# Optimization experiments

Hardware: AMD Instinct MI355X
Metric: run time of the kernel (lower is better)

## Reference

```python
import jax, jax.numpy as jnp
import numpy as np

SEQ, BSZ, D = 1024, 16, 512
HEADS = 8
DEG = 32
N = SEQ * BSZ
E = N * DEG
NEG_SLOPE = 0.2  # PyG GATConv leaky_relu slope


def setup_inputs() -> dict:
    key = jax.random.key(0)
    ks = jax.random.split(key, 12)
    x = jax.random.normal(ks[0], (SEQ, BSZ, D), dtype=jnp.float32)
    # per-graph random COO edges, node ids offset per graph (PyG Batch semantics)
    src = jax.random.randint(ks[1], (BSZ, SEQ * DEG), 0, SEQ)
    dst = jax.random.randint(ks[2], (BSZ, SEQ * DEG), 0, SEQ)
    off = (jnp.arange(BSZ) * SEQ)[:, None]
    edge_index = jnp.stack([(src + off).reshape(-1), (dst + off).reshape(-1)]).astype(jnp.int32)  # [2, E]
    s = 0.05
    W0 = jax.random.normal(ks[3], (D, D), dtype=jnp.float32) * s          # heads*64 = 512
    att_src0 = jax.random.normal(ks[4], (HEADS, 64), dtype=jnp.float32) * s
    att_dst0 = jax.random.normal(ks[5], (HEADS, 64), dtype=jnp.float32) * s
    b0 = jax.random.normal(ks[6], (D,), dtype=jnp.float32) * s
    W1 = jax.random.normal(ks[7], (D, HEADS * D), dtype=jnp.float32) * s  # concat=False layer
    att_src1 = jax.random.normal(ks[8], (HEADS, D), dtype=jnp.float32) * s
    att_dst1 = jax.random.normal(ks[9], (HEADS, D), dtype=jnp.float32) * s
    b1 = jax.random.normal(ks[10], (D,), dtype=jnp.float32) * s
    return {"x": x, "edge_index": edge_index, "W0": W0, "att_src0": att_src0,
            "att_dst0": att_dst0, "b0": b0, "W1": W1, "att_src1": att_src1,
            "att_dst1": att_dst1, "b1": b1}


def gat_conv(h_in, src, dst, n_nodes, W, a_src, a_dst, b, concat):
    """PyG GATConv (eval mode: no dropout). src/dst already include self-loops."""
    H, C = a_src.shape
    h = (h_in @ W).reshape(n_nodes, H, C)                     # [N,H,C]
    alpha_src = jnp.einsum('nhc,hc->nh', h, a_src)            # [N,H]
    alpha_dst = jnp.einsum('nhc,hc->nh', h, a_dst)
    e = jax.nn.leaky_relu(alpha_src[src] + alpha_dst[dst], NEG_SLOPE)  # [Etot,H]
    # segment softmax over incoming edges of each dst node
    m = jax.ops.segment_max(e, dst, num_segments=n_nodes)
    m = jnp.where(jnp.isfinite(m), m, 0.0)
    p = jnp.exp(e - m[dst])
    z = jax.ops.segment_sum(p, dst, num_segments=n_nodes)
    alpha = p / (z[dst] + 1e-16)                              # [Etot,H]
    msg = h[src] * alpha[:, :, None]                          # [Etot,H,C]
    out = jax.ops.segment_sum(msg, dst, num_segments=n_nodes) # [N,H,C]
    out = out.reshape(n_nodes, H * C) if concat else out.mean(axis=1)
    return out + b


def reference(x, edge_index, W0, att_src0, att_dst0, b0, W1, att_src1, att_dst1, b1):
    seq_len, bsz, d = x.shape
    n_nodes = seq_len * bsz
    # PyG Batch: graph n contributes x[:, n, :] as its node block
    nodes = jnp.transpose(x, (1, 0, 2)).reshape(n_nodes, d)
    # GATConv add_self_loops=True
    loop = jnp.arange(n_nodes, dtype=edge_index.dtype)
    src = jnp.concatenate([edge_index[0], loop])
    dst = jnp.concatenate([edge_index[1], loop])
    h = jax.nn.elu(gat_conv(nodes, src, dst, n_nodes, W0, att_src0, att_dst0, b0, concat=True))
    h = jax.nn.elu(gat_conv(h, src, dst, n_nodes, W1, att_src1, att_dst1, b1, concat=False))
    # original code: conv_x.view(seq_len, bsz, embed_dim)  (raw memory reinterpret)
    return h.reshape(seq_len, bsz, d)
```

## Files before the change

### kernel.cpp

```cpp
#include <hip/hip_runtime.h>
#include <hip/hip_bf16.h>


#define NNODES 16384

typedef unsigned short u16;
typedef unsigned int u32;
typedef __attribute__((ext_vector_type(8))) __bf16 bf16x8;
typedef __attribute__((ext_vector_type(4))) float f32x4;

__device__ __forceinline__ u16 f2bf(float v) {
    u32 u = __builtin_bit_cast(u32, v);
    u32 r = (u + 0x7fffu + ((u >> 16) & 1u)) >> 16;
    return (u16)r;
}
__device__ __forceinline__ float bf2f(u16 s) {
    u32 u = ((u32)s) << 16;
    return __builtin_bit_cast(float, u);
}
__device__ __forceinline__ float bflo(u32 u) {
    return __builtin_bit_cast(float, u << 16);
}
__device__ __forceinline__ float bfhi(u32 u) {
    return __builtin_bit_cast(float, u & 0xffff0000u);
}
__device__ __forceinline__ void split2(float v, u16& h, u16& l) {
    h = f2bf(v);
    l = f2bf(v - bf2f(h));
}
__device__ __forceinline__ u32 pack2(float a, float b) {
    return (u32)f2bf(a) | ((u32)f2bf(b) << 16);
}

__device__ __forceinline__ void gload_lds16(const u16* g, u16* l) {
    __builtin_amdgcn_global_load_lds(
        (__attribute__((address_space(1))) void*)(void*)(g),
        (__attribute__((address_space(3))) void*)(void*)(l), 16, 0, 0);
}

__global__ void zero_k(int* p, int n) {
    int i = blockIdx.x * 256 + threadIdx.x;
    if (i < n) p[i] = 0;
}

__global__ void count_k(const int* __restrict__ dst, int E, int* __restrict__ deg) {
    int i = blockIdx.x * 256 + threadIdx.x;
    if (i < E) atomicAdd(&deg[dst[i]], 1);
}

__global__ __launch_bounds__(1024) void scan_k(const int* __restrict__ deg,
                                               int* __restrict__ indptr,
                                               int* __restrict__ cursor, int n) {
    __shared__ int sums[1024];
    int t = threadIdx.x;
    int base = t * 16;
    int local[16];
    int s = 0;
    #pragma unroll
    for (int i = 0; i < 16; i++) { local[i] = s; s += deg[base + i]; }
    sums[t] = s;
    __syncthreads();
    for (int off = 1; off < 1024; off <<= 1) {
        int v = (t >= off) ? sums[t - off] : 0;
        __syncthreads();
        sums[t] += v;
        __syncthreads();
    }
    int base_sum = (t == 0) ? 0 : sums[t - 1];
    #pragma unroll
    for (int i = 0; i < 16; i++) {
        int v = base_sum + local[i];
        indptr[base + i] = v;
        cursor[base + i] = v;
    }
    if (t == 1023) indptr[n] = base_sum + s;
}

__global__ void scatter_k(const int* __restrict__ src, const int* __restrict__ dst,
                          int E, int* __restrict__ cursor, int* __restrict__ csr) {
    int i = blockIdx.x * 256 + threadIdx.x;
    if (i < E) {
        int pos = atomicAdd(&cursor[dst[i]], 1);
        csr[pos] = src[i];
    }
}

__global__ void prepx_k(const float* __restrict__ x, u16* __restrict__ xh,
                        u16* __restrict__ xl) {
    int idx = blockIdx.x * 256 + threadIdx.x;
    int e = idx << 2;
    int n = e >> 9, k = e & 511;
    int g = n >> 10, s = n & 1023;
    float4 v = *(const float4*)(x + ((size_t)(s * 16 + g) << 9) + k);
    u16 h[4], l[4];
    split2(v.x, h[0], l[0]);
    split2(v.y, h[1], l[1]);
    split2(v.z, h[2], l[2]);
    split2(v.w, h[3], l[3]);
    size_t o = ((size_t)n << 9) + k;
    *(ushort4*)(xh + o) = make_ushort4(h[0], h[1], h[2], h[3]);
    *(ushort4*)(xl + o) = make_ushort4(l[0], l[1], l[2], l[3]);
}

__global__ __launch_bounds__(256) void prepW0t_k(const float* __restrict__ W0,
                                                 u16* __restrict__ Wh,
                                                 u16* __restrict__ Wl) {
    __shared__ u32 tile[64][65];
    int b = blockIdx.x;
    int kt = (b >> 3) * 64, nt = (b & 7) * 64;
    int t = threadIdx.x;
    #pragma unroll
    for (int i = 0; i < 16; i++) {
        int idx = i * 256 + t;
        int r = idx >> 6, c = idx & 63;
        float v = W0[(size_t)(kt + r) * 512 + nt + c];
        u16 h, l;
        split2(v, h, l);
        tile[r][c] = ((u32)h << 16) | l;
    }
    __syncthreads();
    #pragma unroll
    for (int i = 0; i < 8; i++) {
        int idx = i * 256 + t;
        int r = idx >> 5, c2 = (idx & 31) * 2;
        u32 p0 = tile[c2][r], p1 = tile[c2 + 1][r];
        size_t o = (size_t)(nt + r) * 512 + kt + c2;
        *(ushort2*)(Wh + o) = make_ushort2((u16)(p0 >> 16), (u16)(p1 >> 16));
        *(ushort2*)(Wl + o) = make_ushort2((u16)(p0 & 0xffff), (u16)(p1 & 0xffff));
    }
}

__global__ __launch_bounds__(256) void prepW1t_k(const float* __restrict__ W1,
                                                 u16* __restrict__ Bh) {
    __shared__ u16 tile[64][66];
    int b = blockIdx.x;
    int hh = b >> 6;
    int rem = b & 63;
    int kt = (rem >> 3) * 64, ct = (rem & 7) * 64;
    int t = threadIdx.x;
    #pragma unroll
    for (int i = 0; i < 16; i++) {
        int idx = i * 256 + t;
        int r = idx >> 6, c = idx & 63;
        float v = W1[(size_t)(kt + r) * 4096 + hh * 512 + ct + c] * 0.125f;
        tile[r][c] = f2bf(v);
    }
    __syncthreads();
    #pragma unroll
    for (int i = 0; i < 8; i++) {
        int idx = i * 256 + t;
        int r = idx >> 5, c2 = (idx & 31) * 2;
        size_t o = (size_t)(ct + r) * 4096 + hh * 512 + kt + c2;
        *(ushort2*)(Bh + o) = make_ushort2(tile[c2][r], tile[c2 + 1][r]);
    }
}

template <int MODE, int TERMS>
__global__ __launch_bounds__(256) void mgemm_k(
    const u16* __restrict__ Ah, const u16* __restrict__ Al,
    const u16* __restrict__ Bh, const u16* __restrict__ Bl,
    void* __restrict__ Cv, int K, const float* __restrict__ bias,
    const float* __restrict__ att_s, const float* __restrict__ att_d,
    float* __restrict__ as_, float* __restrict__ ad_) {
    constexpr int pAl = 4096;
    constexpr int pBh = (TERMS == 3) ? 8192 : 4096;
    constexpr int pBl = 12288;
    constexpr int NSEG = (TERMS == 3) ? 8 : 4;
    __shared__ u16 smem[(TERMS == 3) ? 16384 : 8192];

    int t = threadIdx.x;
    int lane = t & 63, w = t >> 6;
    int wr = w >> 1, wc = w & 1;
    int row0 = blockIdx.y * 128, col0 = blockIdx.x * 128;

    f32x4 acc[4][4];
    #pragma unroll
    for (int i = 0; i < 4; i++)
        #pragma unroll
        for (int j = 0; j < 4; j++) acc[i][j] = (f32x4){0.f, 0.f, 0.f, 0.f};

    int srow = lane >> 2;
    int sl4 = lane & 3;
    const u16* gp[NSEG];
    u16* lp[NSEG];
    #pragma unroll
    for (int ii = 0; ii < NSEG; ii++) {
        int s = w * NSEG + ii;
        int pl = s >> 3, seg = s & 7;
        const u16* gb;
        int g0;
        if (TERMS == 3) {
            gb = (pl == 0) ? Ah : (pl == 1) ? Al : (pl == 2) ? Bh : Bl;
            g0 = (pl < 2) ? row0 : col0;
        } else {
            gb = (pl == 0) ? Ah : Bh;
            g0 = (pl == 0) ? row0 : col0;
        }
        int row = seg * 16 + srow;
        int slot = sl4 ^ ((row >> 1) & 3);
        gp[ii] = gb + (size_t)(g0 + row) * K + slot * 8;
        lp[ii] = smem + pl * 4096 + seg * 512;
    }

    int rl = lane & 15, kb = lane >> 4;

    for (int k0 = 0; k0 < K; k0 += 32) {
        #pragma unroll
        for (int ii = 0; ii < NSEG; ii++) gload_lds16(gp[ii] + k0, lp[ii]);
        __syncthreads();

        bf16x8 afh[4], afl_[4], bfh[4], bfl[4];
        #pragma unroll
        for (int f = 0; f < 4; f++) {
            int r = wr * 64 + f * 16 + rl;
            int off = r * 32 + ((kb ^ ((r >> 1) & 3)) << 3);
            afh[f] = *(const bf16x8*)(smem + off);
            if (TERMS == 3) afl_[f] = *(const bf16x8*)(smem + pAl + off);
        }
        #pragma unroll
        for (int j = 0; j < 4; j++) {
            int r = wc * 64 + j * 16 + rl;
            int off = r * 32 + ((kb ^ ((r >> 1) & 3)) << 3);
            bfh[j] = *(const bf16x8*)(smem + pBh + off);
            if (TERMS == 3) bfl[j] = *(const bf16x8*)(smem + pBl + off);
        }
        #pragma unroll
        for (int i = 0; i < 4; i++)
            #pragma unroll
            for (int j = 0; j < 4; j++) {
                if (TERMS == 3) {
                    acc[i][j] = __builtin_amdgcn_mfma_f32_16x16x32_bf16(
                        afl_[i], bfh[j], acc[i][j], 0, 0, 0);
                    acc[i][j] = __builtin_amdgcn_mfma_f32_16x16x32_bf16(
                        afh[i], bfl[j], acc[i][j], 0, 0, 0);
                }
                acc[i][j] = __builtin_amdgcn_mfma_f32_16x16x32_bf16(
                    afh[i], bfh[j], acc[i][j], 0, 0, 0);
            }
        __syncthreads();
    }

    int cr = kb * 4;
    #pragma unroll
    for (int i = 0; i < 4; i++) {
        #pragma unroll
        for (int j = 0; j < 4; j++) {
            int col = col0 + wc * 64 + j * 16 + rl;
            float bv = (MODE == 1) ? bias[col] : 0.f;
            f32x4 v = acc[i][j];
            #pragma unroll
            for (int q = 0; q < 4; q++) {
                float o = v[q] + bv;
                size_t grow = (size_t)(row0 + wr * 64 + i * 16 + cr + q);
                if (MODE == 1) {
                    o = o > 0.f ? o : __expf(o) - 1.f;
                    ((float*)Cv)[grow * 512 + col] = o;
                } else {
                    ((u16*)Cv)[grow * 512 + col] = f2bf(o);
                }
            }
        }
    }

    if (MODE == 2) {
        int h = (col0 >> 6) + wc;
        float as_v[4], ad_v[4];
        #pragma unroll
        for (int j = 0; j < 4; j++) {
            as_v[j] = att_s[h * 64 + j * 16 + rl];
            ad_v[j] = att_d[h * 64 + j * 16 + rl];
        }
        #pragma unroll
        for (int i = 0; i < 4; i++) {
            float ps[4] = {}, pd[4] = {};
            #pragma unroll
            for (int j = 0; j < 4; j++) {
                f32x4 v = acc[i][j];
                #pragma unroll
                for (int q = 0; q < 4; q++) {
                    ps[q] = fmaf(v[q], as_v[j], ps[q]);
                    pd[q] = fmaf(v[q], ad_v[j], pd[q]);
                }
            }
            #pragma unroll
            for (int off = 1; off < 16; off <<= 1) {
                #pragma unroll
                for (int q = 0; q < 4; q++) {
                    ps[q] += __shfl_xor(ps[q], off);
                    pd[q] += __shfl_xor(pd[q], off);
                }
            }
            if (rl == 0) {
                #pragma unroll
                for (int q = 0; q < 4; q++) {
                    size_t row = (size_t)(row0 + wr * 64 + i * 16 + cr + q);
                    as_[row * 8 + h] = ps[q];
                    ad_[row * 8 + h] = pd[q];
                }
            }
        }
    }
}

__global__ __launch_bounds__(256) void prep1_k(const float* __restrict__ W1,
                                               const float* __restrict__ as1,
                                               const float* __restrict__ ad1,
                                               float* __restrict__ ws1,
                                               float* __restrict__ wd1) {
    int k = blockIdx.x;
    int t = threadIdx.x;
    int h = t >> 5, lane = t & 31;
    float ps = 0.f, pd = 0.f;
    for (int c = lane; c < 512; c += 32) {
        float w = W1[(size_t)k * 4096 + h * 512 + c];
        ps += w * as1[h * 512 + c];
        pd += w * ad1[h * 512 + c];
    }
    #pragma unroll
    for (int off = 1; off < 32; off <<= 1) {
        ps += __shfl_xor(ps, off);
        pd += __shfl_xor(pd, off);
    }
    if (lane == 0) {
        ws1[k * 8 + h] = ps;
        wd1[k * 8 + h] = pd;
    }
}

__global__ __launch_bounds__(256) void node0w_k(
    const u16* __restrict__ h0b, const float* __restrict__ asrc,
    const float* __restrict__ adst, const int* __restrict__ indptr,
    const int* __restrict__ csr, const float* __restrict__ b0,
    const float* __restrict__ ws1, const float* __restrict__ wd1,
    u16* __restrict__ hl0b, float* __restrict__ as1, float* __restrict__ ad1) {
    int b = blockIdx.x;
    int wid = threadIdx.x >> 6;
    int l = threadIdx.x & 63;
    int d = (b & 7) * (NNODES / 8) + ((b >> 3) << 2) + wid;
    int h = l >> 3;
    int e0 = indptr[d];
    int ne = indptr[d + 1] - e0;
    float adh = adst[d * 8 + h];

    float m = -3.0e38f, z = 0.f;
    for (int e = (l & 7); e <= ne; e += 8) {
        int s = (e < ne) ? csr[e0 + e] : d;
        float v = asrc[s * 8 + h] + adh;
        v = v > 0.f ? v : 0.2f * v;
        float mn = fmaxf(m, v);
        z = z * __expf(m - mn) + __expf(v - mn);
        m = mn;
    }
    #pragma unroll
    for (int off = 1; off < 8; off <<= 1) {
        float mo = __shfl_xor(m, off);
        float zo = __shfl_xor(z, off);
        float mn = fmaxf(m, mo);
        z = z * __expf(m - mn) + zo * __expf(mo - mn);
        m = mn;
    }
    float rz = 1.0f / (z + 1e-16f);

    float acc[8] = {};
    for (int eb = 0; eb <= ne; eb += 8) {
        int idx = eb + (l & 7);
        int sv = (idx < ne) ? csr[e0 + idx] : d;
        int nn = min(8, ne + 1 - eb);
        #pragma unroll
        for (int i = 0; i < 8; i++) {
            if (i < nn) {
                int s = __shfl(sv, (l & 56) | i);
                float v = asrc[s * 8 + h] + adh;
                v = v > 0.f ? v : 0.2f * v;
                float a = __expf(v - m) * rz;
                int4 pv = *(const int4*)(h0b + ((size_t)s << 9) + 8 * l);
                acc[0] = fmaf(a, bflo(pv.x), acc[0]);
                acc[1] = fmaf(a, bfhi(pv.x), acc[1]);
                acc[2] = fmaf(a, bflo(pv.y), acc[2]);
                acc[3] = fmaf(a, bfhi(pv.y), acc[3]);
                acc[4] = fmaf(a, bflo(pv.z), acc[4]);
                acc[5] = fmaf(a, bfhi(pv.z), acc[5]);
                acc[6] = fmaf(a, bflo(pv.w), acc[6]);
                acc[7] = fmaf(a, bfhi(pv.w), acc[7]);
            }
        }
    }

    const float4* b4 = (const float4*)(b0 + 8 * l);
    float4 bva = b4[0], bvb = b4[1];
    float o[8];
    o[0] = acc[0] + bva.x; o[1] = acc[1] + bva.y;
    o[2] = acc[2] + bva.z; o[3] = acc[3] + bva.w;
    o[4] = acc[4] + bvb.x; o[5] = acc[5] + bvb.y;
    o[6] = acc[6] + bvb.z; o[7] = acc[7] + bvb.w;
    #pragma unroll
    for (int k = 0; k < 8; k++) o[k] = o[k] > 0.f ? o[k] : __expf(o[k]) - 1.f;
    int4 hv;
    hv.x = (int)pack2(o[0], o[1]);
    hv.y = (int)pack2(o[2], o[3]);
    hv.z = (int)pack2(o[4], o[5]);
    hv.w = (int)pack2(o[6], o[7]);
    *(int4*)(hl0b + ((size_t)d << 9) + 8 * l) = hv;

    float ps[8] = {}, pd[8] = {};
    #pragma unroll
    for (int k = 0; k < 8; k++) {
        const float4* w4 = (const float4*)(ws1 + (size_t)(8 * l + k) * 8);
        const float4* v4 = (const float4*)(wd1 + (size_t)(8 * l + k) * 8);
        float4 wa = w4[0], wb = w4[1];
        float4 va = v4[0], vb = v4[1];
        float ok = o[k];
        ps[0] = fmaf(ok, wa.x, ps[0]); ps[1] = fmaf(ok, wa.y, ps[1]);
        ps[2] = fmaf(ok, wa.z, ps[2]); ps[3] = fmaf(ok, wa.w, ps[3]);
        ps[4] = fmaf(ok, wb.x, ps[4]); ps[5] = fmaf(ok, wb.y, ps[5]);
        ps[6] = fmaf(ok, wb.z, ps[6]); ps[7] = fmaf(ok, wb.w, ps[7]);
        pd[0] = fmaf(ok, va.x, pd[0]); pd[1] = fmaf(ok, va.y, pd[1]);
        pd[2] = fmaf(ok, va.z, pd[2]); pd[3] = fmaf(ok, va.w, pd[3]);
        pd[4] = fmaf(ok, vb.x, pd[4]); pd[5] = fmaf(ok, vb.y, pd[5]);
        pd[6] = fmaf(ok, vb.z, pd[6]); pd[7] = fmaf(ok, vb.w, pd[7]);
    }
    #pragma unroll
    for (int off = 1; off < 64; off <<= 1) {
        #pragma unroll
        for (int j = 0; j < 8; j++) {
            ps[j] += __shfl_xor(ps[j], off);
            pd[j] += __shfl_xor(pd[j], off);
        }
    }
    #pragma unroll
    for (int j = 0; j < 8; j++) {
        if (l == j) as1[(size_t)d * 8 + j] = ps[j];
        if (l == 8 + j) ad1[(size_t)d * 8 + j] = pd[j];
    }
}

__global__ __launch_bounds__(256) void node1w_k(
    const u16* __restrict__ hl0b, const float* __restrict__ asrc,
    const float* __restrict__ adst, const int* __restrict__ indptr,
    const int* __restrict__ csr, u16* __restrict__ aggh, int base, int ch) {
    int b = blockIdx.x;
    int wid = threadIdx.x >> 6;
    int l = threadIdx.x & 63;
    int dl = (b & 7) * (ch >> 3) + ((b >> 3) << 2) + wid;
    int d = base + dl;
    int hme = l & 7;
    int e0 = indptr[d];
    int ne = indptr[d + 1] - e0;
    float adh = adst[d * 8 + hme];

    float m = -3.0e38f, z = 0.f;
    for (int e = (l >> 3); e <= ne; e += 8) {
        int s = (e < ne) ? csr[e0 + e] : d;
        float v = asrc[s * 8 + hme] + adh;
        v = v > 0.f ? v : 0.2f * v;
        float mn = fmaxf(m, v);
        z = z * __expf(m - mn) + __expf(v - mn);
        m = mn;
    }
    #pragma unroll
    for (int off = 8; off < 64; off <<= 1) {
        float mo = __shfl_xor(m, off);
        float zo = __shfl_xor(z, off);
        float mn = fmaxf(m, mo);
        z = z * __expf(m - mn) + zo * __expf(mo - mn);
        m = mn;
    }
    float rz = 1.0f / (z + 1e-16f);

    float acc[8][8] = {};
    for (int eb = 0; eb <= ne; eb += 8) {
        int idx = eb + (l & 7);
        int sv = (idx < ne) ? csr[e0 + idx] : d;
        int nn = min(8, ne + 1 - eb);
        #pragma unroll
        for (int i = 0; i < 8; i++) {
            if (i < nn) {
                int s = __shfl(sv, (l & 56) | i);
                float v = asrc[s * 8 + hme] + adh;
                v = v > 0.f ? v : 0.2f * v;
                float amine = __expf(v - m) * rz;
                float a[8];
                #pragma unroll
                for (int hh = 0; hh < 8; hh++)
                    a[hh] = __shfl(amine, (l & 56) | hh);
                int4 pv = *(const int4*)(hl0b + ((size_t)s << 9) + 8 * l);
                float f0 = bflo(pv.x), f1 = bfhi(pv.x);
                float f2 = bflo(pv.y), f3 = bfhi(pv.y);
                float f4 = bflo(pv.z), f5 = bfhi(pv.z);
                float f6 = bflo(pv.w), f7 = bfhi(pv.w);
                #pragma unroll
                for (int hh = 0; hh < 8; hh++) {
                    acc[hh][0] = fmaf(a[hh], f0, acc[hh][0]);
                    acc[hh][1] = fmaf(a[hh], f1, acc[hh][1]);
                    acc[hh][2] = fmaf(a[hh], f2, acc[hh][2]);
                    acc[hh][3] = fmaf(a[hh], f3, acc[hh][3]);
                    acc[hh][4] = fmaf(a[hh], f4, acc[hh][4]);
                    acc[hh][5] = fmaf(a[hh], f5, acc[hh][5]);
                    acc[hh][6] = fmaf(a[hh], f6, acc[hh][6]);
                    acc[hh][7] = fmaf(a[hh], f7, acc[hh][7]);
                }
            }
        }
    }

    #pragma unroll
    for (int hh = 0; hh < 8; hh++) {
        ushort4 qa = make_ushort4(f2bf(acc[hh][0]), f2bf(acc[hh][1]),
                                  f2bf(acc[hh][2]), f2bf(acc[hh][3]));
        ushort4 qb = make_ushort4(f2bf(acc[hh][4]), f2bf(acc[hh][5]),
                                  f2bf(acc[hh][6]), f2bf(acc[hh][7]));
        size_t ob = (size_t)dl * 4096 + hh * 512 + 8 * l;
        *(ushort4*)(aggh + ob) = qa;
        *(ushort4*)(aggh + ob + 4) = qb;
    }
}

extern "C" void kernel_launch(void* const* d_in, const int* in_sizes, int n_in,
                              void* d_out, int out_size, void* d_ws, size_t ws_size,
                              hipStream_t stream) {
    const float* x = (const float*)d_in[0];
    const int* ei = (const int*)d_in[1];
    const float* W0 = (const float*)d_in[2];
    const float* at_s0 = (const float*)d_in[3];
    const float* at_d0 = (const float*)d_in[4];
    const float* b0 = (const float*)d_in[5];
    const float* W1 = (const float*)d_in[6];
    const float* at_s1 = (const float*)d_in[7];
    const float* at_d1 = (const float*)d_in[8];
    const float* b1 = (const float*)d_in[9];
    float* out = (float*)d_out;

    const int N = NNODES;
    const int E = in_sizes[1] / 2;
    const int* esrc = ei;
    const int* edst = ei + E;

    char* p = (char*)d_ws;
    auto carve = [&](size_t bytes) -> void* {
        void* r = (void*)p;
        p += ((bytes + 255) & ~(size_t)255);
        return r;
    };
    u16* h0b = (u16*)carve((size_t)N * 512 * 2);
    u16* hl0b = (u16*)carve((size_t)N * 512 * 2);
    float* as0 = (float*)carve((size_t)N * 8 * 4);
    float* ad0 = (float*)carve((size_t)N * 8 * 4);
    float* as1 = (float*)carve((size_t)N * 8 * 4);
    float* ad1 = (float*)carve((size_t)N * 8 * 4);
    int* deg = (int*)carve((size_t)N * 4);
    int* indptr = (int*)carve((size_t)(N + 1) * 4);
    int* cursor = (int*)carve((size_t)N * 4);
    int* csr = (int*)carve((size_t)E * 4);
    float* ws1 = (float*)carve(512 * 8 * 4);
    float* wd1 = (float*)carve(512 * 8 * 4);
    u16* xh = (u16*)carve((size_t)N * 512 * 2);
    u16* xl = (u16*)carve((size_t)N * 512 * 2);
    u16* W0h = (u16*)carve((size_t)512 * 512 * 2);
    u16* W0l = (u16*)carve((size_t)512 * 512 * 2);
    u16* B1h = (u16*)carve((size_t)512 * 4096 * 2);
    size_t used = (size_t)(p - (char*)d_ws);

    int CH = 1024;
    const int cands[5] = {16384, 8192, 4096, 2048, 1024};
    for (int ci = 0; ci < 5; ci++) {
        if (ws_size >= used + (size_t)cands[ci] * 8192 + 512) {
            CH = cands[ci];
            break;
        }
    }
    u16* aggh = (u16*)carve((size_t)CH * 4096 * 2);

    zero_k<<<(N + 255) / 256, 256, 0, stream>>>(deg, N);
    count_k<<<(E + 255) / 256, 256, 0, stream>>>(edst, E, deg);
    scan_k<<<1, 1024, 0, stream>>>(deg, indptr, cursor, N);
    scatter_k<<<(E + 255) / 256, 256, 0, stream>>>(esrc, edst, E, cursor, csr);

    prepx_k<<<(N * 512 / 4 + 255) / 256, 256, 0, stream>>>(x, xh, xl);
    prepW0t_k<<<64, 256, 0, stream>>>(W0, W0h, W0l);
    prepW1t_k<<<512, 256, 0, stream>>>(W1, B1h);
    prep1_k<<<512, 256, 0, stream>>>(W1, at_s1, at_d1, ws1, wd1);

    mgemm_k<2, 3><<<dim3(4, N / 128), 256, 0, stream>>>(
        xh, xl, W0h, W0l, h0b, 512, nullptr, at_s0, at_d0, as0, ad0);
    node0w_k<<<N / 4, 256, 0, stream>>>(h0b, as0, ad0, indptr, csr, b0, ws1,
                                        wd1, hl0b, as1, ad1);

    for (int base = 0; base < N; base += CH) {
        node1w_k<<<CH / 4, 256, 0, stream>>>(hl0b, as1, ad1, indptr, csr, aggh,
                                             base, CH);
        mgemm_k<1, 1><<<dim3(4, CH / 128), 256, 0, stream>>>(
            aggh, nullptr, B1h, nullptr, out + (size_t)base * 512, 4096, b1,
            nullptr, nullptr, nullptr, nullptr);
    }
}
```

Measured before the change: 441.5 us.

## Remap GEMM blocks per XCD and double K-step for single-term path

The block index is remapped so that consecutive row-tiles land on the same XCD, with four column tiles sharing an A row-panel, to improve L2 reuse of A across the chiplet caches. The single-term (TERMS==1) path now loads 64 K-columns per iteration into the full 32KB shared buffer, halving the number of barriers and load rounds per tile. The remapping assumes gridDim.x==4 and gridDim.y divisible by 8. It also raises LDS use for the single-term kernel, which may reduce occupancy.

```diff
diff --git a/kernel.cpp b/kernel.cpp
--- a/kernel.cpp
+++ b/kernel.cpp
@@ -162,16 +162,17 @@
     void* __restrict__ Cv, int K, const float* __restrict__ bias,
     const float* __restrict__ att_s, const float* __restrict__ att_d,
     float* __restrict__ as_, float* __restrict__ ad_) {
-    constexpr int pAl = 4096;
-    constexpr int pBh = (TERMS == 3) ? 8192 : 4096;
-    constexpr int pBl = 12288;
-    constexpr int NSEG = (TERMS == 3) ? 8 : 4;
-    __shared__ u16 smem[(TERMS == 3) ? 16384 : 8192];
+    __shared__ u16 smem[16384];
 
     int t = threadIdx.x;
     int lane = t & 63, w = t >> 6;
     int wr = w >> 1, wc = w & 1;
-    int row0 = blockIdx.y * 128, col0 = blockIdx.x * 128;
+
+    int orig = blockIdx.x + (blockIdx.y << 2);
+    int xcd = orig & 7, slot = orig >> 3;
+    int by = xcd * ((int)gridDim.y >> 3) + (slot >> 2);
+    int bx = slot & 3;
+    int row0 = by * 128, col0 = bx * 128;
 
     f32x4 acc[4][4];
     #pragma unroll
@@ -181,63 +182,93 @@
 
     int srow = lane >> 2;
     int sl4 = lane & 3;
-    const u16* gp[NSEG];
-    u16* lp[NSEG];
-    #pragma unroll
-    for (int ii = 0; ii < NSEG; ii++) {
-        int s = w * NSEG + ii;
-        int pl = s >> 3, seg = s & 7;
+    const u16* gp[8];
+    u16* lp[8];
+    #pragma unroll
+    for (int ii = 0; ii < 8; ii++) {
         const u16* gb;
-        int g0;
+        int g0, koff;
         if (TERMS == 3) {
-            gb = (pl == 0) ? Ah : (pl == 1) ? Al : (pl == 2) ? Bh : Bl;
-            g0 = (pl < 2) ? row0 : col0;
+            gb = (w == 0) ? Ah : (w == 1) ? Al : (w == 2) ? Bh : Bl;
+            g0 = (w < 2) ? row0 : col0;
+            koff = 0;
         } else {
-            gb = (pl == 0) ? Ah : Bh;
-            g0 = (pl == 0) ? row0 : col0;
-        }
-        int row = seg * 16 + srow;
-        int slot = sl4 ^ ((row >> 1) & 3);
-        gp[ii] = gb + (size_t)(g0 + row) * K + slot * 8;
-        lp[ii] = smem + pl * 4096 + seg * 512;
+            gb = (w < 2) ? Ah : Bh;
+            g0 = (w < 2) ? row0 : col0;
+            koff = (w & 1) * 32;
+        }
+        int row = ii * 16 + srow;
+        int sslot = sl4 ^ ((row >> 1) & 3);
+        gp[ii] = gb + (size_t)(g0 + row) * K + koff + sslot * 8;
+        lp[ii] = smem + w * 4096 + ii * 512;
     }
 
     int rl = lane & 15, kb = lane >> 4;
 
-    for (int k0 = 0; k0 < K; k0 += 32) {
-        #pragma unroll
-        for (int ii = 0; ii < NSEG; ii++) gload_lds16(gp[ii] + k0, lp[ii]);
-        __syncthreads();
-
-        bf16x8 afh[4], afl_[4], bfh[4], bfl[4];
-        #pragma unroll
-        for (int f = 0; f < 4; f++) {
-            int r = wr * 64 + f * 16 + rl;
-            int off = r * 32 + ((kb ^ ((r >> 1) & 3)) << 3);
-            afh[f] = *(const bf16x8*)(smem + off);
-            if (TERMS == 3) afl_[f] = *(const bf16x8*)(smem + pAl + off);
-        }
-        #pragma unroll
-        for (int j = 0; j < 4; j++) {
-            int r = wc * 64 + j * 16 + rl;
-            int off = r * 32 + ((kb ^ ((r >> 1) & 3)) << 3);
-            bfh[j] = *(const bf16x8*)(smem + pBh + off);
-            if (TERMS == 3) bfl[j] = *(const bf16x8*)(smem + pBl + off);
-        }
-        #pragma unroll
-        for (int i = 0; i < 4; i++)
+    if (TERMS == 3) {
+        for (int k0 = 0; k0 < K; k0 += 32) {
+            #pragma unroll
+            for (int ii = 0; ii < 8; ii++) gload_lds16(gp[ii] + k0, lp[ii]);
+            __syncthreads();
+
+            bf16x8 afh[4], afl_[4], bfh[4], bfl[4];
+            #pragma unroll
+            for (int f = 0; f < 4; f++) {
+                int r = wr * 64 + f * 16 + rl;
+                int off = r * 32 + ((kb ^ ((r >> 1) & 3)) << 3);
+                afh[f] = *(const bf16x8*)(smem + off);
+                afl_[f] = *(const bf16x8*)(smem + 4096 + off);
+            }
             #pragma unroll
             for (int j = 0; j < 4; j++) {
-                if (TERMS == 3) {
+                int r = wc * 64 + j * 16 + rl;
+                int off = r * 32 + ((kb ^ ((r >> 1) & 3)) << 3);
+                bfh[j] = *(const bf16x8*)(smem + 8192 + off);
+                bfl[j] = *(const bf16x8*)(smem + 12288 + off);
+            }
+            #pragma unroll
+            for (int i = 0; i < 4; i++)
+                #pragma unroll
+                for (int j = 0; j < 4; j++) {
                     acc[i][j] = __builtin_amdgcn_mfma_f32_16x16x32_bf16(
                         afl_[i], bfh[j], acc[i][j], 0, 0, 0);
                     acc[i][j] = __builtin_amdgcn_mfma_f32_16x16x32_bf16(
                         afh[i], bfl[j], acc[i][j], 0, 0, 0);
-                }
-                acc[i][j] = __builtin_amdgcn_mfma_f32_16x16x32_bf16(
-                    afh[i], bfh[j], acc[i][j], 0, 0, 0);
-            }
-        __syncthreads();
+                    acc[i][j] = __builtin_amdgcn_mfma_f32_16x16x32_bf16(
+                        afh[i], bfh[j], acc[i][j], 0, 0, 0);
+                }
+            __syncthreads();
+        }
+    } else {
+        for (int k0 = 0; k0 < K; k0 += 64) {
+            #pragma unroll
+            for (int ii = 0; ii < 8; ii++) gload_lds16(gp[ii] + k0, lp[ii]);
+            __syncthreads();
+
+            #pragma unroll
+            for (int ks = 0; ks < 2; ks++) {
+                bf16x8 af[4], bf[4];
+                #pragma unroll
+                for (int f = 0; f < 4; f++) {
+                    int r = wr * 64 + f * 16 + rl;
+                    int off = r * 32 + ((kb ^ ((r >> 1) & 3)) << 3);
+                    af[f] = *(const bf16x8*)(smem + ks * 4096 + off);
+                }
+                #pragma unroll
+                for (int j = 0; j < 4; j++) {
+                    int r = wc * 64 + j * 16 + rl;
+                    int off = r * 32 + ((kb ^ ((r >> 1) & 3)) << 3);
+                    bf[j] = *(const bf16x8*)(smem + 8192 + ks * 4096 + off);
+                }
+                #pragma unroll
+                for (int i = 0; i < 4; i++)
+                    #pragma unroll
+                    for (int j = 0; j < 4; j++)
+                        acc[i][j] = __builtin_amdgcn_mfma_f32_16x16x32_bf16(
+                            af[i], bf[j], acc[i][j], 0, 0, 0);
+            }
+            __syncthreads();
+        }
     }
 
     int cr = kb * 4;
```

Result: faster. 402.5 us (-8.8%).
